# Performance work log

Hardware: AMD Instinct MI355X
Metric: run time of the kernel (lower is better)

Reference implementation:

```python
import jax, jax.numpy as jnp
import numpy as np

N = 4096      # num_nodes
F = 16        # num_features
K = 3         # diffusion steps


def _diffusion_powers(W):
    """Replicates __init__: powers of (DO^-1 W) and (DI^-1 W^T), k=0..K-1."""
    out_deg = W.sum(axis=1)            # W @ ones
    in_deg = W.sum(axis=0)             # W.T @ ones
    A = W / out_deg[:, None]           # DO_inv @ W
    B = W.T / in_deg[:, None]          # DI_inv @ W.T
    eye = jnp.eye(N, dtype=W.dtype)
    Wp, WTp, Pa, Pb = [], [], eye, eye
    for _ in range(K):
        Wp.append(Pa)
        WTp.append(Pb)
        Pa = Pa @ A
        Pb = Pb @ B
    return jnp.stack(Wp), jnp.stack(WTp)   # each [K, N, N]


def setup_inputs() -> dict:
    key = jax.random.key(0)
    k1, k2, k3 = jax.random.split(key, 3)
    W = jax.random.uniform(k1, (N, N), dtype=jnp.float32)  # random adjacency, like np.random.rand
    Wp, WTp = _diffusion_powers(W)
    X = jax.random.normal(k2, (N, F), dtype=jnp.float32)
    theta = jax.random.normal(k3, (K, 2), dtype=jnp.float32)
    return {"X": X, "theta": theta, "Wp": Wp, "WTp": WTp}


def reference(X, theta, Wp, WTp):
    # Original: for each feature p and step k,
    #   X_out[:, p] += (theta[k,0]*Wp[k] + theta[k,1]*WTp[k]) @ X[:, p]
    # The feature loop is a columnwise matmul; fuse the k-sum into one matrix M.
    M = jnp.einsum('k,knm->nm', theta[:, 0], Wp) + jnp.einsum('k,knm->nm', theta[:, 1], WTp)
    return X + M @ X
```

## Files before the change

kernel.cpp:

```cpp
#include <hip/hip_runtime.h>


constexpr int N  = 4096;
constexpr int F  = 16;
constexpr int TM = 8;
constexpr int TK = 128;

__global__ __launch_bounds__(256) void diffconv_kernel(
    const float* __restrict__ X,
    const float* __restrict__ theta,
    const float* __restrict__ Wp,
    const float* __restrict__ WTp,
    float* __restrict__ out)
{
    __shared__ float c_lds[TM][TK];
    __shared__ float x_lds[TK][F];
    __shared__ float red_lds[4][TM][F];

    const int t    = threadIdx.x;
    const int row0 = blockIdx.x * TM;

    const float th10 = theta[2], th11 = theta[3];
    const float th20 = theta[4], th21 = theta[5];
    const float self_scale = 1.0f + theta[0] + theta[1];

    const float* __restrict__ Wp1  = Wp  + (size_t)N * N;
    const float* __restrict__ Wp2  = Wp  + 2 * (size_t)N * N;
    const float* __restrict__ WTp1 = WTp + (size_t)N * N;
    const float* __restrict__ WTp2 = WTp + 2 * (size_t)N * N;

    const int sr = t >> 5;
    const int sc = (t & 31) << 2;

    const int f0 = (t & 3) << 2;
    const int m0 = (t >> 2) << 1;

    float acc[TM][4];
#pragma unroll
    for (int r = 0; r < TM; ++r)
#pragma unroll
        for (int j = 0; j < 4; ++j) acc[r][j] = 0.0f;

    for (int kb = 0; kb < N; kb += TK) {
        const size_t moff = (size_t)(row0 + sr) * N + (size_t)(kb + sc);
        float4 a0 = *(const float4*)(Wp1  + moff);
        float4 a1 = *(const float4*)(WTp1 + moff);
        float4 a2 = *(const float4*)(Wp2  + moff);
        float4 a3 = *(const float4*)(WTp2 + moff);
        float4 c4;
        c4.x = th10*a0.x + th11*a1.x + th20*a2.x + th21*a3.x;
        c4.y = th10*a0.y + th11*a1.y + th20*a2.y + th21*a3.y;
        c4.z = th10*a0.z + th11*a1.z + th20*a2.z + th21*a3.z;
        c4.w = th10*a0.w + th11*a1.w + th20*a2.w + th21*a3.w;
        *(float4*)&c_lds[sr][sc] = c4;

#pragma unroll
        for (int i = 0; i < 2; ++i) {
            const int idx = t + i * 256;
            const int xr  = idx >> 2;
            const int xc  = (idx & 3) << 2;
            *(float4*)&x_lds[xr][xc] =
                *(const float4*)(X + (size_t)(kb + xr) * F + xc);
        }
        __syncthreads();

        const float4 x0 = *(const float4*)&x_lds[m0][f0];
        const float4 x1 = *(const float4*)&x_lds[m0 + 1][f0];
#pragma unroll
        for (int r = 0; r < TM; ++r) {
            const float2 c = *(const float2*)&c_lds[r][m0];
            acc[r][0] = fmaf(c.x, x0.x, fmaf(c.y, x1.x, acc[r][0]));
            acc[r][1] = fmaf(c.x, x0.y, fmaf(c.y, x1.y, acc[r][1]));
            acc[r][2] = fmaf(c.x, x0.z, fmaf(c.y, x1.z, acc[r][2]));
            acc[r][3] = fmaf(c.x, x0.w, fmaf(c.y, x1.w, acc[r][3]));
        }
        __syncthreads();
    }

#pragma unroll
    for (int mask = 4; mask <= 32; mask <<= 1) {
#pragma unroll
        for (int r = 0; r < TM; ++r)
#pragma unroll
            for (int j = 0; j < 4; ++j)
                acc[r][j] += __shfl_xor(acc[r][j], mask, 64);
    }

    const int wave = t >> 6;
    const int lane = t & 63;
    if (lane < 4) {
#pragma unroll
        for (int r = 0; r < TM; ++r)
#pragma unroll
            for (int j = 0; j < 4; ++j)
                red_lds[wave][r][lane * 4 + j] = acc[r][j];
    }
    __syncthreads();

    if (t < TM * F) {
        const int r = t >> 4;
        const int f = t & 15;
        const float s = red_lds[0][r][f] + red_lds[1][r][f]
                      + red_lds[2][r][f] + red_lds[3][r][f];
        const int row = row0 + r;
        out[(size_t)row * F + f] = fmaf(self_scale, X[(size_t)row * F + f], s);
    }
}

extern "C" void kernel_launch(void* const* d_in, const int* in_sizes, int n_in,
                              void* d_out, int out_size, void* d_ws, size_t ws_size,
                              hipStream_t stream) {
    const float* X     = (const float*)d_in[0];
    const float* theta = (const float*)d_in[1];
    const float* Wp    = (const float*)d_in[2];
    const float* WTp   = (const float*)d_in[3];
    float* out = (float*)d_out;

    diffconv_kernel<<<N / TM, 256, 0, stream>>>(X, theta, Wp, WTp, out);
}
```

Before: 371.6 us.

## Split K across blocks with atomic reduction and register-prefetch next tile

Splits the reduction dimension across four blocks per row tile, giving four times as many blocks, and combines their partial sums with atomicAdd into an output that a separate init kernel first fills with the scaled X term. Global loads for the next K tile are issued into registers before the compute on the current tile, so the two overlap within a single shared buffer. The X tile in LDS is padded to reduce bank conflicts. The changes add a second kernel launch and atomic traffic, and make the floating-point summation order nondeterministic.

```diff
diff --git a/kernel.cpp b/kernel.cpp
--- a/kernel.cpp
+++ b/kernel.cpp
@@ -5,6 +5,22 @@
 constexpr int F  = 16;
 constexpr int TM = 8;
 constexpr int TK = 128;
+constexpr int KS = 4;
+constexpr int XP = F + 4;
+
+__global__ __launch_bounds__(256) void init_out_kernel(
+    const float* __restrict__ X,
+    const float* __restrict__ theta,
+    float* __restrict__ out)
+{
+    const float self_scale = 1.0f + theta[0] + theta[1];
+    const int i = blockIdx.x * blockDim.x + threadIdx.x;
+    if (i < N * F / 4) {
+        float4 x = ((const float4*)X)[i];
+        x.x *= self_scale; x.y *= self_scale; x.z *= self_scale; x.w *= self_scale;
+        ((float4*)out)[i] = x;
+    }
+}
 
 __global__ __launch_bounds__(256) void diffconv_kernel(
     const float* __restrict__ X,
@@ -14,15 +30,15 @@
     float* __restrict__ out)
 {
     __shared__ float c_lds[TM][TK];
-    __shared__ float x_lds[TK][F];
+    __shared__ float x_lds[TK][XP];
     __shared__ float red_lds[4][TM][F];
 
     const int t    = threadIdx.x;
     const int row0 = blockIdx.x * TM;
+    const int kbeg = blockIdx.y * (N / KS);
 
     const float th10 = theta[2], th11 = theta[3];
     const float th20 = theta[4], th21 = theta[5];
-    const float self_scale = 1.0f + theta[0] + theta[1];
 
     const float* __restrict__ Wp1  = Wp  + (size_t)N * N;
     const float* __restrict__ Wp2  = Wp  + 2 * (size_t)N * N;
@@ -31,6 +47,11 @@
 
     const int sr = t >> 5;
     const int sc = (t & 31) << 2;
+
+    const int xr0 = t >> 2;
+    const int xc0 = (t & 3) << 2;
+    const int xr1 = (t + 256) >> 2;
+    const int xc1 = xc0;
 
     const int f0 = (t & 3) << 2;
     const int m0 = (t >> 2) << 1;
@@ -41,28 +62,37 @@
 #pragma unroll
         for (int j = 0; j < 4; ++j) acc[r][j] = 0.0f;
 
-    for (int kb = 0; kb < N; kb += TK) {
-        const size_t moff = (size_t)(row0 + sr) * N + (size_t)(kb + sc);
-        float4 a0 = *(const float4*)(Wp1  + moff);
-        float4 a1 = *(const float4*)(WTp1 + moff);
-        float4 a2 = *(const float4*)(Wp2  + moff);
-        float4 a3 = *(const float4*)(WTp2 + moff);
+    constexpr int NIT = N / KS / TK;
+
+    size_t moff = (size_t)(row0 + sr) * N + (size_t)(kbeg + sc);
+    float4 a0 = *(const float4*)(Wp1  + moff);
+    float4 a1 = *(const float4*)(WTp1 + moff);
+    float4 a2 = *(const float4*)(Wp2  + moff);
+    float4 a3 = *(const float4*)(WTp2 + moff);
+    float4 xv0 = *(const float4*)(X + (size_t)(kbeg + xr0) * F + xc0);
+    float4 xv1 = *(const float4*)(X + (size_t)(kbeg + xr1) * F + xc1);
+
+    for (int it = 0; it < NIT; ++it) {
         float4 c4;
         c4.x = th10*a0.x + th11*a1.x + th20*a2.x + th21*a3.x;
         c4.y = th10*a0.y + th11*a1.y + th20*a2.y + th21*a3.y;
         c4.z = th10*a0.z + th11*a1.z + th20*a2.z + th21*a3.z;
         c4.w = th10*a0.w + th11*a1.w + th20*a2.w + th21*a3.w;
         *(float4*)&c_lds[sr][sc] = c4;
+        *(float4*)&x_lds[xr0][xc0] = xv0;
+        *(float4*)&x_lds[xr1][xc1] = xv1;
+        __syncthreads();
 
-#pragma unroll
-        for (int i = 0; i < 2; ++i) {
-            const int idx = t + i * 256;
-            const int xr  = idx >> 2;
-            const int xc  = (idx & 3) << 2;
-            *(float4*)&x_lds[xr][xc] =
-                *(const float4*)(X + (size_t)(kb + xr) * F + xc);
+        if (it + 1 < NIT) {
+            const int kb = kbeg + (it + 1) * TK;
+            moff = (size_t)(row0 + sr) * N + (size_t)(kb + sc);
+            a0 = *(const float4*)(Wp1  + moff);
+            a1 = *(const float4*)(WTp1 + moff);
+            a2 = *(const float4*)(Wp2  + moff);
+            a3 = *(const float4*)(WTp2 + moff);
+            xv0 = *(const float4*)(X + (size_t)(kb + xr0) * F + xc0);
+            xv1 = *(const float4*)(X + (size_t)(kb + xr1) * F + xc1);
         }
-        __syncthreads();
 
         const float4 x0 = *(const float4*)&x_lds[m0][f0];
         const float4 x1 = *(const float4*)&x_lds[m0 + 1][f0];
@@ -102,8 +132,7 @@
         const int f = t & 15;
         const float s = red_lds[0][r][f] + red_lds[1][r][f]
                       + red_lds[2][r][f] + red_lds[3][r][f];
-        const int row = row0 + r;
-        out[(size_t)row * F + f] = fmaf(self_scale, X[(size_t)row * F + f], s);
+        atomicAdd(&out[(size_t)(row0 + r) * F + f], s);
     }
 }
 
@@ -116,5 +145,8 @@
     const float* WTp   = (const float*)d_in[3];
     float* out = (float*)d_out;
 
-    diffconv_kernel<<<N / TM, 256, 0, stream>>>(X, theta, Wp, WTp, out);
+    init_out_kernel<<<(N * F / 4 + 255) / 256, 256, 0, stream>>>(X, theta, out);
+
+    dim3 grid(N / TM, KS);
+    diffconv_kernel<<<grid, 256, 0, stream>>>(X, theta, Wp, WTp, out);
 }
```

Result: no change. 366.6 us (-1.3%).
